# Optimization experiments

Hardware: AMD Instinct MI355X
Metric: run time of the kernel (lower is better)

The kernel has to match this reference:

```python
import jax
import jax.numpy as jnp
from jax import lax
import numpy as np

B, C, H, W = 32, 256, 56, 56
GROUPS = 4
EPS = 1e-5


@jax.custom_vjp
def binarize(x):
    # Conv2d_1w1a: sign binarization with straight-through estimator (clip |x|<=1)
    return jnp.sign(x)

def _bin_fwd(x):
    return jnp.sign(x), x

def _bin_bwd(x, g):
    return (g * (jnp.abs(x) <= 1.0).astype(g.dtype),)

binarize.defvjp(_bin_fwd, _bin_bwd)


def batchnorm(x, gamma, beta):
    # BatchNorm2d in training mode: per-channel batch statistics over (N,H,W)
    mean = jnp.mean(x, axis=(0, 2, 3), keepdims=True)
    var = jnp.var(x, axis=(0, 2, 3), keepdims=True)
    inv = lax.rsqrt(var + EPS)
    return (x - mean) * inv * gamma[None, :, None, None] + beta[None, :, None, None]


def setup_inputs() -> dict:
    key = jax.random.key(0)
    k1, k2, k3 = jax.random.split(key, 3)
    x = jax.random.normal(k1, (B, C, H, W), dtype=jnp.float32)
    # grouped 3x3 conv weight: [C_out, C_in/groups, kH, kW]
    w1 = jax.random.normal(k2, (C, C // GROUPS, 3, 3), dtype=jnp.float32) * 0.05
    # 1x1 conv weight
    w2 = jax.random.normal(k3, (C, C, 1, 1), dtype=jnp.float32) * 0.05
    g1 = jnp.ones((C,), jnp.float32)
    b1 = jnp.zeros((C,), jnp.float32)
    g2 = jnp.ones((C,), jnp.float32)
    b2 = jnp.zeros((C,), jnp.float32)
    return {"x": x, "w1": w1, "g1": g1, "b1": b1, "w2": w2, "g2": g2, "b2": b2}


def reference(x, w1, g1, b1, w2, g2, b2):
    dn = ("NCHW", "OIHW", "NCHW")
    # conv_1: binary grouped 3x3, stride 2, pad 1, dilation 1
    out = lax.conv_general_dilated(
        binarize(x), binarize(w1),
        window_strides=(2, 2), padding=[(1, 1), (1, 1)],
        dimension_numbers=dn, feature_group_count=GROUPS)
    out = batchnorm(out, g1, b1)
    # shortcut (options='C'): MaxPool2d(kernel=3, stride=2, padding=1)
    sc = lax.reduce_window(
        x, -jnp.inf, lax.max,
        window_dimensions=(1, 1, 3, 3), window_strides=(1, 1, 2, 2),
        padding=[(0, 0), (0, 0), (1, 1), (1, 1)])
    out = out + sc
    x1 = out
    # conv_2: binary 1x1
    out = lax.conv_general_dilated(
        binarize(out), binarize(w2),
        window_strides=(1, 1), padding=[(0, 0), (0, 0)],
        dimension_numbers=dn)
    out = batchnorm(out, g2, b2)
    out = out + x1
    return out
```

## Files before the change

kernel.cpp:

```cpp
#include <hip/hip_runtime.h>
#include <cstdint>
#include <math.h>

#define NB 32
#define NC 256
#define NH 56
#define NW 56
#define OHH 28
#define OWW 28
#define NG 4
#define EPSV 1e-5

static constexpr int HW   = NH * NW;
static constexpr int OHW  = OHH * OWW;
static constexpr int NOUT = NB * NC * OHW;
static constexpr int NRED = NB * OHW;
static constexpr int NQ   = NRED / 4;
static constexpr int QW   = OHW / 4;
static constexpr int PTILE = 56;

#define TAU1 2e-5f

__global__ void pack_x_k(const float* __restrict__ x,
                         unsigned long long* __restrict__ xbits) {
    int idx = blockIdx.x * blockDim.x + threadIdx.x;
    int wq = idx % (NW / 4);
    int h  = (idx / (NW / 4)) % NH;
    int g  = (idx / (NW / 4 * NH)) % NG;
    int b  = idx / (NW / 4 * NH * NG);
    const float* xp = x + (((size_t)b * NC + g * 64) * NH + h) * NW + wq * 4;
    unsigned long long b0 = 0, b1 = 0, b2 = 0, b3 = 0;
#pragma unroll
    for (int ci = 0; ci < 64; ++ci) {
        float4 v = *(const float4*)(xp + (size_t)ci * HW);
        b0 |= (unsigned long long)(v.x >= 0.0f) << ci;
        b1 |= (unsigned long long)(v.y >= 0.0f) << ci;
        b2 |= (unsigned long long)(v.z >= 0.0f) << ci;
        b3 |= (unsigned long long)(v.w >= 0.0f) << ci;
    }
    unsigned long long* dst = xbits + ((size_t)(b * NG + g) * NH + h) * NW + wq * 4;
    dst[0] = b0; dst[1] = b1; dst[2] = b2; dst[3] = b3;
}

__global__ void pack_w_k(const float* __restrict__ w1,
                         const float* __restrict__ w2,
                         unsigned long long* __restrict__ wbits,
                         unsigned long long* __restrict__ w2bits) {
    int idx = blockIdx.x * blockDim.x + threadIdx.x;
    if (idx < 2304) {
        int tap = idx % 9;
        int co  = idx / 9;
        const float* wp = w1 + (size_t)co * 64 * 9 + tap;
        unsigned long long bits = 0;
#pragma unroll
        for (int ci = 0; ci < 64; ++ci)
            bits |= (unsigned long long)(wp[ci * 9] >= 0.0f) << ci;
        wbits[idx] = bits;
    } else {
        int i2 = idx - 2304;
        int k  = i2 % 4;
        int co = i2 / 4;
        const float* p = w2 + (size_t)co * 256 + k * 64;
        unsigned long long bits = 0;
#pragma unroll
        for (int ci = 0; ci < 64; ++ci)
            bits |= (unsigned long long)(p[ci] >= 0.0f) << ci;
        w2bits[i2] = bits;
    }
}

__global__ void __launch_bounds__(448) conv1_lds(
        const unsigned long long* __restrict__ xbits,
        const unsigned long long* __restrict__ wbits,
        short* __restrict__ y1) {
    int blk = blockIdx.x;
    int ohq = blk & 3;
    int g   = (blk >> 2) & 3;
    int b   = blk >> 4;
    int tid = threadIdx.x;
    int co  = tid & 63;
    int ohl = tid >> 6;

    __shared__ unsigned long long xs[15 * 57];
    __shared__ short ybuf[64][198];

    int ih0 = ohq * 14 - 1;
    const unsigned long long* xb = xbits + (size_t)(b * NG + g) * HW;
    for (int i = tid; i < 15 * 57; i += 448) {
        int r  = i / 57;
        int cc = i % 57;
        int ih = ih0 + r;
        unsigned long long v = 0;
        if (cc > 0 && (unsigned)ih < (unsigned)NH) v = xb[ih * NW + (cc - 1)];
        xs[i] = v;
    }
    __syncthreads();

    int coG = g * 64 + co;
    const unsigned long long* wb = wbits + coG * 9;
    unsigned long long w0 = wb[0], w1 = wb[1], w2 = wb[2],
                       w3 = wb[3], w4 = wb[4], w5 = wb[5],
                       w6 = wb[6], w7 = wb[7], w8 = wb[8];
    int oh = ohq * 7 + ohl;
    int t0 = 64 - 2 * __popcll(w0), t1 = 64 - 2 * __popcll(w1), t2 = 64 - 2 * __popcll(w2);
    int t3 = 64 - 2 * __popcll(w3), t6 = 64 - 2 * __popcll(w6);
    int base9   = 576 - ((oh == 0) ? (t0 + t1 + t2) : 0);
    int colcorr = t3 + t6 + ((oh == 0) ? 0 : t0);

    const unsigned long long* r0 = xs + (ohl * 2 + 0) * 57;
    const unsigned long long* r1 = xs + (ohl * 2 + 1) * 57;
    const unsigned long long* r2 = xs + (ohl * 2 + 2) * 57;
    short* yrow = &ybuf[co][ohl * 28];
    for (int ow = 0; ow < OWW; ++ow) {
        int cbase = ow * 2;
        int acc = __popcll(r0[cbase] ^ w0) + __popcll(r0[cbase + 1] ^ w1) + __popcll(r0[cbase + 2] ^ w2)
                + __popcll(r1[cbase] ^ w3) + __popcll(r1[cbase + 1] ^ w4) + __popcll(r1[cbase + 2] ^ w5)
                + __popcll(r2[cbase] ^ w6) + __popcll(r2[cbase + 1] ^ w7) + __popcll(r2[cbase + 2] ^ w8);
        int y = base9 - ((ow == 0) ? colcorr : 0) - 2 * acc;
        yrow[ow] = (short)y;
    }
    __syncthreads();

    for (int i = tid; i < 64 * 196; i += 448) {
        int c2 = i / 196;
        int j  = i % 196;
        y1[((size_t)(b * NC + g * 64 + c2) * OHH + ohq * 7) * OWW + j] =
            ybuf[c2][j];
    }
}

__global__ void stats_k(const short* __restrict__ src,
                        const float* __restrict__ gamma,
                        const float* __restrict__ beta,
                        double vdiv,
                        double* __restrict__ scale,
                        double* __restrict__ shift) {
    int c   = blockIdx.x;
    int tid = threadIdx.x;
    long long sum = 0, sumsq = 0;
    for (int p = tid; p < NQ; p += 512) {
        int b = p / QW;
        int q = p % QW;
        short4 v = *(const short4*)&src[((size_t)b * NC + c) * OHW + q * 4];
        sum   += (long long)v.x + v.y + v.z + v.w;
        sumsq += (long long)v.x * v.x + (long long)v.y * v.y +
                 (long long)v.z * v.z + (long long)v.w * v.w;
    }
    __shared__ long long s1[512];
    __shared__ long long s2[512];
    s1[tid] = sum; s2[tid] = sumsq;
    __syncthreads();
    for (int st = 256; st > 0; st >>= 1) {
        if (tid < st) { s1[tid] += s1[tid + st]; s2[tid] += s2[tid + st]; }
        __syncthreads();
    }
    if (tid == 0) {
        double n    = (double)NRED;
        double mean = (double)s1[0] / (n * vdiv);
        double var  = (double)s2[0] / (n * vdiv * vdiv) - mean * mean;
        double inv  = 1.0 / sqrt(var + EPSV);
        double sc   = (double)gamma[c] * inv;
        scale[c] = sc;
        shift[c] = (double)beta[c] - mean * sc;
    }
}

__global__ void __launch_bounds__(256) x1_lds(
        const short* __restrict__ y1,
        const float* __restrict__ x,
        const double* __restrict__ scale,
        const double* __restrict__ shift,
        float* __restrict__ out) {
    int blk = blockIdx.x;
    int c   = blk & 255;
    int tid = threadIdx.x;
    __shared__ float xs[HW];
    const float4* xp4 = (const float4*)(x + (size_t)blk * HW);
    float4* xs4 = (float4*)xs;
    for (int i = tid; i < HW / 4; i += 256) xs4[i] = xp4[i];
    __syncthreads();
    double sc = scale[c], sh = shift[c];
    const short* yp = y1 + (size_t)blk * OHW;
    float* op = out + (size_t)blk * OHW;
    for (int s = tid; s < OHW; s += 256) {
        int oh = s / OWW, ow = s % OWW;
        float m = -3.4e38f;
#pragma unroll
        for (int kh = 0; kh < 3; ++kh) {
            int ih = oh * 2 - 1 + kh;
            if ((unsigned)ih >= (unsigned)NH) continue;
#pragma unroll
            for (int kw = 0; kw < 3; ++kw) {
                int iw = ow * 2 - 1 + kw;
                if ((unsigned)iw >= (unsigned)NW) continue;
                m = fmaxf(m, xs[ih * NW + iw]);
            }
        }
        op[s] = (float)((double)yp[s] * sc + sh + (double)m);
    }
}

__global__ void __launch_bounds__(256) conv2f_lds(
        const float* __restrict__ x1,
        const unsigned long long* __restrict__ w2bits,
        short* __restrict__ z2) {
    int blk  = blockIdx.x;
    int t    = blk % 14;
    int b    = blk / 14;
    int tid  = threadIdx.x;
    int lane = tid & 63;
    int w    = tid >> 6;
    int s0   = t * PTILE;
    __shared__ float xs[NC][PTILE + 1];
    __shared__ unsigned long long bitsL[4][PTILE];
    __shared__ unsigned long long hedgeL[4][PTILE];

    {
        const float4* src = (const float4*)(x1 + ((size_t)b * NC + tid) * OHW + s0);
        float* dst = xs[tid];
#pragma unroll
        for (int q = 0; q < 14; ++q) {
            float4 v = src[q];
            dst[q * 4 + 0] = v.x; dst[q * 4 + 1] = v.y;
            dst[q * 4 + 2] = v.z; dst[q * 4 + 3] = v.w;
        }
    }
    __syncthreads();

    for (int px = 0; px < PTILE; ++px) {
        float v = xs[w * 64 + lane][px];
        unsigned long long bb = __ballot(v >= 0.0f);
        unsigned long long hh = __ballot(fabsf(v) < TAU1);
        if (lane == 0) { bitsL[w][px] = bb; hedgeL[w][px] = hh; }
    }
    __syncthreads();

    for (int it = 0; it < 64; ++it) {
        int co = it * 4 + w;
        const unsigned long long* wb = w2bits + co * 4;
        unsigned long long wv0 = wb[0], wv1 = wb[1], wv2 = wb[2], wv3 = wb[3];
        if (lane < PTILE) {
            unsigned long long d0 = bitsL[0][lane] ^ wv0, d1 = bitsL[1][lane] ^ wv1,
                               d2 = bitsL[2][lane] ^ wv2, d3 = bitsL[3][lane] ^ wv3;
            unsigned long long h0 = hedgeL[0][lane], h1 = hedgeL[1][lane],
                               h2 = hedgeL[2][lane], h3 = hedgeL[3][lane];
            int full = 256 - 2 * (__popcll(d0) + __popcll(d1) + __popcll(d2) + __popcll(d3));
            int hcorr = __popcll(h0) + __popcll(h1) + __popcll(h2) + __popcll(h3)
                      - 2 * (__popcll(h0 & d0) + __popcll(h1 & d1) +
                             __popcll(h2 & d2) + __popcll(h3 & d3));
            z2[((size_t)b * NC + co) * OHW + s0 + lane] = (short)(2 * full - hcorr);
        }
    }
}

__global__ void final_k(const short* __restrict__ z2,
                        const double* __restrict__ scale,
                        const double* __restrict__ shift,
                        float* __restrict__ out) {
    int idx = blockIdx.x * blockDim.x + threadIdx.x;
    int c = (idx / QW) % NC;
    short4 zz = ((const short4*)z2)[idx];
    float4 o  = ((const float4*)out)[idx];
    double sc = scale[c], sh = shift[c];
    o.x = (float)((double)zz.x * 0.5 * sc + sh + (double)o.x);
    o.y = (float)((double)zz.y * 0.5 * sc + sh + (double)o.y);
    o.z = (float)((double)zz.z * 0.5 * sc + sh + (double)o.z);
    o.w = (float)((double)zz.w * 0.5 * sc + sh + (double)o.w);
    ((float4*)out)[idx] = o;
}

extern "C" void kernel_launch(void* const* d_in, const int* in_sizes, int n_in,
                              void* d_out, int out_size, void* d_ws, size_t ws_size,
                              hipStream_t stream) {
    const float* x  = (const float*)d_in[0];
    const float* w1 = (const float*)d_in[1];
    const float* g1 = (const float*)d_in[2];
    const float* b1 = (const float*)d_in[3];
    const float* w2 = (const float*)d_in[4];
    const float* g2 = (const float*)d_in[5];
    const float* b2 = (const float*)d_in[6];
    float* out = (float*)d_out;

    char* ws = (char*)d_ws;
    auto alloc = [&](size_t bytes) -> char* {
        char* p = ws;
        ws += (bytes + 255) & ~(size_t)255;
        return p;
    };

    unsigned long long* xbits   = (unsigned long long*)alloc((size_t)NB * NG * HW * 8);
    unsigned long long* wbits1  = (unsigned long long*)alloc((size_t)NC * 9 * 8);
    unsigned long long* w2bits  = (unsigned long long*)alloc((size_t)NC * 4 * 8);
    short*              y1      = (short*)alloc((size_t)NOUT * 2);
    short*              z2buf   = (short*)alloc((size_t)NOUT * 2);
    double*             scale1  = (double*)alloc(NC * 8);
    double*             shift1  = (double*)alloc(NC * 8);
    double*             scale2  = (double*)alloc(NC * 8);
    double*             shift2  = (double*)alloc(NC * 8);

    const int T = 256;

    pack_x_k  <<<(NB * NG * HW / 4) / T, T, 0, stream>>>(x, xbits);
    pack_w_k  <<<13,                     T, 0, stream>>>(w1, w2, wbits1, w2bits);
    conv1_lds <<<NB * NG * 4,          448, 0, stream>>>(xbits, wbits1, y1);
    stats_k   <<<NC,                   512, 0, stream>>>(y1, g1, b1, 1.0, scale1, shift1);
    x1_lds    <<<NB * NC,                T, 0, stream>>>(y1, x, scale1, shift1, out);
    conv2f_lds<<<NB * 14,                T, 0, stream>>>(out, w2bits, z2buf);
    stats_k   <<<NC,                   512, 0, stream>>>(z2buf, g2, b2, 2.0, scale2, shift2);
    final_k   <<<(NOUT / 4) / T,         T, 0, stream>>>(z2buf, scale2, shift2, out);
}
```

Measured before the change: 126.8 us.

## Fuse max-pool into bit-packing pass so x is read from HBM once

The sign-packing kernel now streams x through a three-row LDS ring buffer, emitting packed channel bits via wave ballot and also computing the 3x3 stride-2 max-pool into a new pooled buffer. The x1 kernel becomes a simple vectorised elementwise combine of y1, pooled and the BN scale/shift, instead of rereading the full 102MB x tensor. This trades a second full read of x for a write and read of a pooled buffer a quarter its size. The fused kernel launches only 512 blocks that loop serially over rows with two barriers per row, which may limit parallelism.

```diff
diff --git a/kernel.cpp b/kernel.cpp
--- a/kernel.cpp
+++ b/kernel.cpp
@@ -21,25 +21,69 @@
 
 #define TAU1 2e-5f
 
-__global__ void pack_x_k(const float* __restrict__ x,
-                         unsigned long long* __restrict__ xbits) {
-    int idx = blockIdx.x * blockDim.x + threadIdx.x;
-    int wq = idx % (NW / 4);
-    int h  = (idx / (NW / 4)) % NH;
-    int g  = (idx / (NW / 4 * NH)) % NG;
-    int b  = idx / (NW / 4 * NH * NG);
-    const float* xp = x + (((size_t)b * NC + g * 64) * NH + h) * NW + wq * 4;
-    unsigned long long b0 = 0, b1 = 0, b2 = 0, b3 = 0;
-#pragma unroll
-    for (int ci = 0; ci < 64; ++ci) {
-        float4 v = *(const float4*)(xp + (size_t)ci * HW);
-        b0 |= (unsigned long long)(v.x >= 0.0f) << ci;
-        b1 |= (unsigned long long)(v.y >= 0.0f) << ci;
-        b2 |= (unsigned long long)(v.z >= 0.0f) << ci;
-        b3 |= (unsigned long long)(v.w >= 0.0f) << ci;
-    }
-    unsigned long long* dst = xbits + ((size_t)(b * NG + g) * NH + h) * NW + wq * 4;
-    dst[0] = b0; dst[1] = b1; dst[2] = b2; dst[3] = b3;
+__global__ void __launch_bounds__(256) pool_pack_k(
+        const float* __restrict__ x,
+        unsigned long long* __restrict__ xbits,
+        float* __restrict__ pooled) {
+    int blk = blockIdx.x;
+    int q   = blk & 3;
+    int g   = (blk >> 2) & 3;
+    int b   = blk >> 4;
+    int tid = threadIdx.x;
+    int lane = tid & 63;
+    int w    = tid >> 6;
+
+    __shared__ float ring[3][64][57];
+
+    const float* xg = x + ((size_t)b * NC + g * 64) * HW;
+    unsigned long long* xbg = xbits + (size_t)(b * NG + g) * HW;
+    float* pg = pooled + ((size_t)b * NC + g * 64) * OHW;
+
+    int ih_lo = q * 14 - 1;
+    int ih_hi = q * 14 + 13;
+    for (int ih = ih_lo; ih <= ih_hi; ++ih) {
+        __syncthreads();
+        int r = (ih + 3) % 3;
+        if (ih >= 0) {
+            for (int i = tid; i < 64 * 14; i += 256) {
+                int ch = i / 14, qq = i % 14;
+                float4 v = *(const float4*)(xg + (size_t)ch * HW + ih * NW + qq * 4);
+                float* d = &ring[r][ch][qq * 4];
+                d[0] = v.x; d[1] = v.y; d[2] = v.z; d[3] = v.w;
+            }
+        }
+        __syncthreads();
+        if (ih >= q * 14) {
+            for (int j = 0; j < 14; ++j) {
+                int px = w * 14 + j;
+                unsigned long long bits = __ballot(ring[r][lane][px] >= 0.0f);
+                if (lane == 0) xbg[ih * NW + px] = bits;
+            }
+        }
+        if ((ih & 1) && ih >= q * 14 + 1) {
+            int oh = (ih - 1) >> 1;
+            int ra = (ih + 1) % 3;
+            int rb = (ih + 2) % 3;
+            int rc = (ih + 3) % 3;
+            for (int i = tid; i < 64 * 28; i += 256) {
+                int ch = i / 28, ow = i % 28;
+                float m = -3.4e38f;
+                int cl = 2 * ow - 1;
+                if (oh > 0) {
+                    if (ow > 0) m = fmaxf(m, ring[ra][ch][cl]);
+                    m = fmaxf(m, ring[ra][ch][cl + 1]);
+                    m = fmaxf(m, ring[ra][ch][cl + 2]);
+                }
+                if (ow > 0) m = fmaxf(m, ring[rb][ch][cl]);
+                m = fmaxf(m, ring[rb][ch][cl + 1]);
+                m = fmaxf(m, ring[rb][ch][cl + 2]);
+                if (ow > 0) m = fmaxf(m, ring[rc][ch][cl]);
+                m = fmaxf(m, ring[rc][ch][cl + 1]);
+                m = fmaxf(m, ring[rc][ch][cl + 2]);
+                pg[(size_t)ch * OHW + oh * OWW + ow] = m;
+            }
+        }
+    }
 }
 
 __global__ void pack_w_k(const float* __restrict__ w1,
@@ -165,39 +209,22 @@
     }
 }
 
-__global__ void __launch_bounds__(256) x1_lds(
-        const short* __restrict__ y1,
-        const float* __restrict__ x,
-        const double* __restrict__ scale,
-        const double* __restrict__ shift,
-        float* __restrict__ out) {
-    int blk = blockIdx.x;
-    int c   = blk & 255;
-    int tid = threadIdx.x;
-    __shared__ float xs[HW];
-    const float4* xp4 = (const float4*)(x + (size_t)blk * HW);
-    float4* xs4 = (float4*)xs;
-    for (int i = tid; i < HW / 4; i += 256) xs4[i] = xp4[i];
-    __syncthreads();
+__global__ void x1_k(const short* __restrict__ y1,
+                     const float* __restrict__ pooled,
+                     const double* __restrict__ scale,
+                     const double* __restrict__ shift,
+                     float* __restrict__ out) {
+    int idx = blockIdx.x * blockDim.x + threadIdx.x;
+    int c = (idx / QW) % NC;
+    short4 yy = ((const short4*)y1)[idx];
+    float4 mm = ((const float4*)pooled)[idx];
     double sc = scale[c], sh = shift[c];
-    const short* yp = y1 + (size_t)blk * OHW;
-    float* op = out + (size_t)blk * OHW;
-    for (int s = tid; s < OHW; s += 256) {
-        int oh = s / OWW, ow = s % OWW;
-        float m = -3.4e38f;
-#pragma unroll
-        for (int kh = 0; kh < 3; ++kh) {
-            int ih = oh * 2 - 1 + kh;
-            if ((unsigned)ih >= (unsigned)NH) continue;
-#pragma unroll
-            for (int kw = 0; kw < 3; ++kw) {
-                int iw = ow * 2 - 1 + kw;
-                if ((unsigned)iw >= (unsigned)NW) continue;
-                m = fmaxf(m, xs[ih * NW + iw]);
-            }
-        }
-        op[s] = (float)((double)yp[s] * sc + sh + (double)m);
-    }
+    float4 o;
+    o.x = (float)((double)yy.x * sc + sh + (double)mm.x);
+    o.y = (float)((double)yy.y * sc + sh + (double)mm.y);
+    o.z = (float)((double)yy.z * sc + sh + (double)mm.z);
+    o.w = (float)((double)yy.w * sc + sh + (double)mm.w);
+    ((float4*)out)[idx] = o;
 }
 
 __global__ void __launch_bounds__(256) conv2f_lds(
@@ -293,6 +320,7 @@
     unsigned long long* w2bits  = (unsigned long long*)alloc((size_t)NC * 4 * 8);
     short*              y1      = (short*)alloc((size_t)NOUT * 2);
     short*              z2buf   = (short*)alloc((size_t)NOUT * 2);
+    float*              pooled  = (float*)alloc((size_t)NOUT * 4);
     double*             scale1  = (double*)alloc(NC * 8);
     double*             shift1  = (double*)alloc(NC * 8);
     double*             scale2  = (double*)alloc(NC * 8);
@@ -300,12 +328,12 @@
 
     const int T = 256;
 
-    pack_x_k  <<<(NB * NG * HW / 4) / T, T, 0, stream>>>(x, xbits);
-    pack_w_k  <<<13,                     T, 0, stream>>>(w1, w2, wbits1, w2bits);
-    conv1_lds <<<NB * NG * 4,          448, 0, stream>>>(xbits, wbits1, y1);
-    stats_k   <<<NC,                   512, 0, stream>>>(y1, g1, b1, 1.0, scale1, shift1);
-    x1_lds    <<<NB * NC,                T, 0, stream>>>(y1, x, scale1, shift1, out);
-    conv2f_lds<<<NB * 14,                T, 0, stream>>>(out, w2bits, z2buf);
-    stats_k   <<<NC,                   512, 0, stream>>>(z2buf, g2, b2, 2.0, scale2, shift2);
-    final_k   <<<(NOUT / 4) / T,         T, 0, stream>>>(z2buf, scale2, shift2, out);
-}
+    pool_pack_k<<<NB * NG * 4,      T, 0, stream>>>(x, xbits, pooled);
+    pack_w_k   <<<13,               T, 0, stream>>>(w1, w2, wbits1, w2bits);
+    conv1_lds  <<<NB * NG * 4,    448, 0, stream>>>(xbits, wbits1, y1);
+    stats_k    <<<NC,             512, 0, stream>>>(y1, g1, b1, 1.0, scale1, shift1);
+    x1_k       <<<(NOUT / 4) / T,   T, 0, stream>>>(y1, pooled, scale1, shift1, out);
+    conv2f_lds <<<NB * 14,          T, 0, stream>>>(out, w2bits, z2buf);
+    stats_k    <<<NC,             512, 0, stream>>>(z2buf, g2, b2, 2.0, scale2, shift2);
+    final_k    <<<(NOUT / 4) / T,   T, 0, stream>>>(z2buf, scale2, shift2, out);
+}
```

Result: slower. 150.8 us (+18.9%).
